# Kernel optimization log

Measured on AMD Instinct MI355X. Metric: run time of the kernel, lower is better.

## Reference

```python
import jax, jax.numpy as jnp
import numpy as np

N = 50000      # nodes
E = 1600000    # edges (avg degree 32)
D_IN = 128
HID = 64


def setup_inputs() -> dict:
    key = jax.random.key(0)
    ks = jax.random.split(key, 7)
    x = jax.random.normal(ks[0], (N, D_IN), dtype=jnp.float32)
    ei = jax.random.randint(ks[1], (2, E), 0, N, dtype=jnp.int32)
    ew = jax.random.uniform(ks[2], (E,), dtype=jnp.float32)
    # GCNConv linear weights (glorot-ish scale); lin has no bias, conv bias added post-aggregation
    W1 = jax.random.normal(ks[3], (HID, D_IN), dtype=jnp.float32) * (1.0 / np.sqrt(D_IN))
    b1 = jnp.zeros((HID,), dtype=jnp.float32)
    W2 = jax.random.normal(ks[4], (HID, HID), dtype=jnp.float32) * (1.0 / np.sqrt(HID))
    b2 = jnp.zeros((HID,), dtype=jnp.float32)
    return {"x": x, "ei": ei, "ew": ew, "W1": W1, "b1": b1, "W2": W2, "b2": b2}


def _gcn_conv(x, src, dst, ew_all, W, b, n_nodes):
    """PyG GCNConv: gcn_norm (self-loops already appended) + x@W.T, gather-scale-scatter, +b."""
    deg = jax.ops.segment_sum(ew_all, dst, num_segments=n_nodes)  # dst-side weighted degree
    dinv = jnp.where(deg > 0, jax.lax.rsqrt(deg), 0.0)            # deg^{-1/2}, inf->0
    norm = dinv[src] * ew_all * dinv[dst]                          # [E+N]
    h = x @ W.T                                                    # [N, hid]
    msg = h[src] * norm[:, None]                                   # gather + scale
    out = jax.ops.segment_sum(msg, dst, num_segments=n_nodes)     # scatter-add
    return out + b


def reference(x, ei, ew, W1, b1, W2, b2):
    n_nodes = x.shape[0]
    # add self loops once (fill value 1.0), shared by both conv layers
    loop = jnp.arange(n_nodes, dtype=ei.dtype)
    src = jnp.concatenate([ei[0], loop])
    dst = jnp.concatenate([ei[1], loop])
    ew_all = jnp.concatenate([ew, jnp.ones((n_nodes,), dtype=ew.dtype)])

    h1 = jax.nn.relu(_gcn_conv(x, src, dst, ew_all, W1, b1, n_nodes))
    # dropout is identity in eval mode
    h2 = _gcn_conv(h1, src, dst, ew_all, W2, b2, n_nodes)
    return h2 + h1
```

## Files before the change

### kernel.cpp

```cpp
#include <hip/hip_runtime.h>

#define HID 64
#define DIN 128
#define NBLK 512
#define CSH 14
#define CAP (1 << CSH)

typedef unsigned long long ull;
typedef unsigned short u16;

static __device__ __forceinline__ u16 f2bf(float f) {
  unsigned u = __float_as_uint(f);
  unsigned lsb = (u >> 16) & 1u;
  u += 0x7fffu + lsb;
  return (u16)(u >> 16);
}


__global__ __launch_bounds__(512) void k_build(const int* __restrict__ src,
                                               const int* __restrict__ dst,
                                               const float* __restrict__ ew,
                                               int* __restrict__ cursor,
                                               int2* __restrict__ bufA,
                                               int E, int NBC, int chunk,
                                               const float* __restrict__ W1,
                                               const float* __restrict__ W2,
                                               float* __restrict__ WT1,
                                               float* __restrict__ WT2) {
  int b = blockIdx.x, tid = threadIdx.x;
  if (b >= NBLK) {
    int idx = (b - NBLK) * 512 + tid;
    if (idx < DIN * 64) {
      int d = idx >> 6, j = idx & 63;
      WT1[idx] = W1[j * DIN + d];
    }
    int i2 = idx - DIN * 64;
    if (i2 >= 0 && i2 < HID * 64) {
      int d = i2 >> 6, j = i2 & 63;
      WT2[i2] = W2[j * HID + d];
    }
    return;
  }
  __shared__ int h[256];
  __shared__ int cur[256];
  if (tid < 256) h[tid] = 0;
  __syncthreads();
  int e0 = b * chunk, e1 = min(E, e0 + chunk);
  for (int e = e0 + tid; e < e1; e += 512) atomicAdd(&h[dst[e] >> 8], 1);
  __syncthreads();
  if (tid < 256) {
    int c = h[tid];
    int ofs = (c > 0) ? atomicAdd(&cursor[tid], c) : 0;
    cur[tid] = (tid << CSH) + ofs;
  }
  __syncthreads();
  for (int e = e0 + tid; e < e1; e += 512) {
    int s = src[e], d = dst[e];
    float w = ew[e];
    int p = atomicAdd(&cur[d >> 8], 1);
    bufA[p] = make_int2(__float_as_int(w), (int)(((unsigned)s << 16) | (unsigned)d));
  }
}


__global__ __launch_bounds__(512) void k_passB(const int2* __restrict__ bufA,
                                               const int* __restrict__ cursor,
                                               int2* __restrict__ bufB,
                                               int* __restrict__ offs,
                                               int* __restrict__ cnt,
                                               float* __restrict__ dinv,
                                               int NBC, int N) {
  int bin = blockIdx.x, tid = threadIdx.x;
  __shared__ int h2[256];
  __shared__ int cur[256];
  __shared__ float dg[256];
  int bbase = bin << CSH;
  int m = cursor[bin];
  if (tid < 256) { h2[tid] = 0; dg[tid] = 0.f; }
  __syncthreads();
  for (int i = tid; i < m; i += 512) {
    unsigned sd = (unsigned)bufA[bbase + i].y;
    atomicAdd(&h2[sd & 255], 1);
  }
  __syncthreads();
  int own = (tid < 256) ? h2[tid] : 0;
  for (int o = 1; o < 256; o <<= 1) {
    int u = 0;
    if (tid < 256 && tid >= o) u = h2[tid - o];
    __syncthreads();
    if (tid < 256) h2[tid] += u;
    __syncthreads();
  }
  int nd = (bin << 8) + tid;
  if (tid < 256) {
    int excl = h2[tid] - own;
    cur[tid] = excl;
    if (nd < N) { offs[nd] = bbase + excl; cnt[nd] = own; }
  }
  __syncthreads();
  for (int i = tid; i < m; i += 512) {
    int2 r = bufA[bbase + i];
    unsigned sd = (unsigned)r.y;
    int dl = (int)(sd & 255u);
    int p = atomicAdd(&cur[dl], 1);
    bufB[bbase + p] = r;
    atomicAdd(&dg[dl], __int_as_float(r.x));
  }
  __syncthreads();
  if (tid < 256 && nd < N) dinv[nd] = rsqrtf(1.0f + dg[tid]);
}


__global__ __launch_bounds__(256) void k_norm(int2* __restrict__ recs,
                                              const int* __restrict__ cursor,
                                              const float* __restrict__ dinv, int nslab) {
  int e = blockIdx.x * 256 + threadIdx.x;
  if (e < nslab && (e & (CAP - 1)) < cursor[e >> CSH]) {
    int2 r = recs[e];
    unsigned sd = (unsigned)r.y;
    int s = (int)(sd >> 16), d = (int)(sd & 0xffffu);
    float nrm = dinv[s] * __int_as_float(r.x) * dinv[d];
    recs[e] = make_int2(__float_as_int(nrm), s);
  }
}


template <int K>
__global__ __launch_bounds__(256) void k_gemm(const float* __restrict__ X,
                                              const float* __restrict__ WTg,
                                              u16* __restrict__ out, int n_nodes) {
  constexpr int PAD = 68;
  __shared__ float XT[64 * PAD];
  __shared__ float WL[64 * PAD];
  const int tid = threadIdx.x;
  const int n0 = blockIdx.x * 64;
  const int tx = tid & 15;
  const int ty = tid >> 4;
  float acc[4][4] = {{0.f}};

  for (int ph = 0; ph < K / 64; ++ph) {
    const int d0 = ph * 64;
    __syncthreads();
#pragma unroll
    for (int k = 0; k < 4; ++k) {
      int f = tid + k * 256;
      int r = f >> 4, q = f & 15;
      int n = n0 + r;
      float4 xv = (n < n_nodes)
        ? *reinterpret_cast<const float4*>(&X[(size_t)n * K + d0 + 4 * q])
        : make_float4(0.f, 0.f, 0.f, 0.f);
      *reinterpret_cast<float4*>(&XT[r * PAD + 4 * q]) = xv;
      float4 wv = *reinterpret_cast<const float4*>(&WTg[(size_t)(d0 + r) * 64 + 4 * q]);
      *reinterpret_cast<float4*>(&WL[r * PAD + 4 * q]) = wv;
    }
    __syncthreads();
#pragma unroll 4
    for (int dd = 0; dd < 64; dd += 4) {
      float4 xs[4], ws[4];
#pragma unroll
      for (int mi = 0; mi < 4; ++mi)
        xs[mi] = *reinterpret_cast<const float4*>(&XT[(4 * ty + mi) * PAD + dd]);
#pragma unroll
      for (int dk = 0; dk < 4; ++dk)
        ws[dk] = *reinterpret_cast<const float4*>(&WL[(dd + dk) * PAD + 4 * tx]);
#pragma unroll
      for (int mi = 0; mi < 4; ++mi) {
        float xm[4] = {xs[mi].x, xs[mi].y, xs[mi].z, xs[mi].w};
#pragma unroll
        for (int dk = 0; dk < 4; ++dk) {
          acc[mi][0] = fmaf(xm[dk], ws[dk].x, acc[mi][0]);
          acc[mi][1] = fmaf(xm[dk], ws[dk].y, acc[mi][1]);
          acc[mi][2] = fmaf(xm[dk], ws[dk].z, acc[mi][2]);
          acc[mi][3] = fmaf(xm[dk], ws[dk].w, acc[mi][3]);
        }
      }
    }
  }

#pragma unroll
  for (int mi = 0; mi < 4; ++mi) {
    int n = n0 + 4 * ty + mi;
    if (n < n_nodes) {
      ushort4 o = make_ushort4(f2bf(acc[mi][0]), f2bf(acc[mi][1]),
                               f2bf(acc[mi][2]), f2bf(acc[mi][3]));
      *reinterpret_cast<ushort4*>(&out[(size_t)n * HID + 4 * tx]) = o;
    }
  }
}


__device__ __forceinline__ void bfma8(const uint4& v, float w, float* a) {
  a[0] = fmaf(__uint_as_float(v.x << 16), w, a[0]);
  a[1] = fmaf(__uint_as_float(v.x & 0xffff0000u), w, a[1]);
  a[2] = fmaf(__uint_as_float(v.y << 16), w, a[2]);
  a[3] = fmaf(__uint_as_float(v.y & 0xffff0000u), w, a[3]);
  a[4] = fmaf(__uint_as_float(v.z << 16), w, a[4]);
  a[5] = fmaf(__uint_as_float(v.z & 0xffff0000u), w, a[5]);
  a[6] = fmaf(__uint_as_float(v.w << 16), w, a[6]);
  a[7] = fmaf(__uint_as_float(v.w & 0xffff0000u), w, a[7]);
}

__global__ __launch_bounds__(256) void k_agg(const u16* __restrict__ h,
                                             const int2* __restrict__ recs,
                                             const int* __restrict__ offs,
                                             const int* __restrict__ cnt,
                                             const float* __restrict__ dinv,
                                             const float* __restrict__ bias,
                                             const float* __restrict__ resid,
                                             float* __restrict__ out, int n_nodes, int mode) {
  int tid = threadIdx.x;
  int lane = tid & 63;
  int g = lane >> 3;
  int p8 = (lane & 7) * 8;
  int node = (blockIdx.x * 4 + (tid >> 6)) * 8 + g;
  if (node >= n_nodes) return;
  int beg = offs[node], end = beg + cnt[node];
  float di = dinv[node];

  float a[8], b[8];
  {
    uint4 v = *reinterpret_cast<const uint4*>(&h[(size_t)node * HID + p8]);
    float w = di * di;
    a[0] = __uint_as_float(v.x << 16) * w;
    a[1] = __uint_as_float(v.x & 0xffff0000u) * w;
    a[2] = __uint_as_float(v.y << 16) * w;
    a[3] = __uint_as_float(v.y & 0xffff0000u) * w;
    a[4] = __uint_as_float(v.z << 16) * w;
    a[5] = __uint_as_float(v.z & 0xffff0000u) * w;
    a[6] = __uint_as_float(v.w << 16) * w;
    a[7] = __uint_as_float(v.w & 0xffff0000u) * w;
#pragma unroll
    for (int j = 0; j < 8; ++j) b[j] = 0.f;
  }

  int i = beg;
  while (i + 8 <= end) {
    int2 r0 = recs[i];     int2 r1 = recs[i + 1];
    int2 r2 = recs[i + 2]; int2 r3 = recs[i + 3];
    int2 r4 = recs[i + 4]; int2 r5 = recs[i + 5];
    int2 r6 = recs[i + 6]; int2 r7 = recs[i + 7];
    uint4 v0 = *reinterpret_cast<const uint4*>(&h[(size_t)r0.y * HID + p8]);
    uint4 v1 = *reinterpret_cast<const uint4*>(&h[(size_t)r1.y * HID + p8]);
    uint4 v2 = *reinterpret_cast<const uint4*>(&h[(size_t)r2.y * HID + p8]);
    uint4 v3 = *reinterpret_cast<const uint4*>(&h[(size_t)r3.y * HID + p8]);
    uint4 v4 = *reinterpret_cast<const uint4*>(&h[(size_t)r4.y * HID + p8]);
    uint4 v5 = *reinterpret_cast<const uint4*>(&h[(size_t)r5.y * HID + p8]);
    uint4 v6 = *reinterpret_cast<const uint4*>(&h[(size_t)r6.y * HID + p8]);
    uint4 v7 = *reinterpret_cast<const uint4*>(&h[(size_t)r7.y * HID + p8]);
    bfma8(v0, __int_as_float(r0.x), a);
    bfma8(v1, __int_as_float(r1.x), b);
    bfma8(v2, __int_as_float(r2.x), a);
    bfma8(v3, __int_as_float(r3.x), b);
    bfma8(v4, __int_as_float(r4.x), a);
    bfma8(v5, __int_as_float(r5.x), b);
    bfma8(v6, __int_as_float(r6.x), a);
    bfma8(v7, __int_as_float(r7.x), b);
    i += 8;
  }
  if (i + 4 <= end) {
    int2 r0 = recs[i];     int2 r1 = recs[i + 1];
    int2 r2 = recs[i + 2]; int2 r3 = recs[i + 3];
    uint4 v0 = *reinterpret_cast<const uint4*>(&h[(size_t)r0.y * HID + p8]);
    uint4 v1 = *reinterpret_cast<const uint4*>(&h[(size_t)r1.y * HID + p8]);
    uint4 v2 = *reinterpret_cast<const uint4*>(&h[(size_t)r2.y * HID + p8]);
    uint4 v3 = *reinterpret_cast<const uint4*>(&h[(size_t)r3.y * HID + p8]);
    bfma8(v0, __int_as_float(r0.x), a);
    bfma8(v1, __int_as_float(r1.x), b);
    bfma8(v2, __int_as_float(r2.x), a);
    bfma8(v3, __int_as_float(r3.x), b);
    i += 4;
  }
  if (i + 2 <= end) {
    int2 r0 = recs[i];     int2 r1 = recs[i + 1];
    uint4 v0 = *reinterpret_cast<const uint4*>(&h[(size_t)r0.y * HID + p8]);
    uint4 v1 = *reinterpret_cast<const uint4*>(&h[(size_t)r1.y * HID + p8]);
    bfma8(v0, __int_as_float(r0.x), a);
    bfma8(v1, __int_as_float(r1.x), b);
    i += 2;
  }
  if (i < end) {
    int2 r0 = recs[i];
    uint4 v0 = *reinterpret_cast<const uint4*>(&h[(size_t)r0.y * HID + p8]);
    bfma8(v0, __int_as_float(r0.x), a);
  }

  float r[8];
#pragma unroll
  for (int j = 0; j < 8; ++j) r[j] = a[j] + b[j];
  float4 bb0 = *reinterpret_cast<const float4*>(&bias[p8]);
  float4 bb1 = *reinterpret_cast<const float4*>(&bias[p8 + 4]);
  r[0] += bb0.x; r[1] += bb0.y; r[2] += bb0.z; r[3] += bb0.w;
  r[4] += bb1.x; r[5] += bb1.y; r[6] += bb1.z; r[7] += bb1.w;
  if (mode == 0) {
#pragma unroll
    for (int j = 0; j < 8; ++j) r[j] = fmaxf(r[j], 0.f);
  } else {
    float4 rs0 = *reinterpret_cast<const float4*>(&resid[(size_t)node * HID + p8]);
    float4 rs1 = *reinterpret_cast<const float4*>(&resid[(size_t)node * HID + p8 + 4]);
    r[0] += rs0.x; r[1] += rs0.y; r[2] += rs0.z; r[3] += rs0.w;
    r[4] += rs1.x; r[5] += rs1.y; r[6] += rs1.z; r[7] += rs1.w;
  }
  *reinterpret_cast<float4*>(&out[(size_t)node * HID + p8]) =
      make_float4(r[0], r[1], r[2], r[3]);
  *reinterpret_cast<float4*>(&out[(size_t)node * HID + p8 + 4]) =
      make_float4(r[4], r[5], r[6], r[7]);
}


extern "C" void kernel_launch(void* const* d_in, const int* in_sizes, int n_in,
                              void* d_out, int out_size, void* d_ws, size_t ws_size,
                              hipStream_t stream) {
  const float* x  = (const float*)d_in[0];
  const int*   ei = (const int*)d_in[1];
  const float* ew = (const float*)d_in[2];
  const float* W1 = (const float*)d_in[3];
  const float* b1 = (const float*)d_in[4];
  const float* W2 = (const float*)d_in[5];
  const float* b2 = (const float*)d_in[6];
  float* out = (float*)d_out;

  const int N = in_sizes[0] / DIN;
  const int E = in_sizes[2];
  const int* src = ei;
  const int* dst = ei + E;

  const int NBC = (N + 255) >> 8;
  const int chunk = (E + NBLK - 1) / NBLK;
  const int nslab = NBC << CSH;

  char* p = (char*)d_ws;
  auto carve = [&](size_t bytes) {
    char* r = p;
    p += (bytes + 255) & ~(size_t)255;
    return r;
  };
  int*   cursor = (int*)carve(256 * 4);
  int*   offs   = (int*)carve((size_t)N * 4);
  int*   cnt    = (int*)carve((size_t)N * 4);
  float* dinv   = (float*)carve((size_t)N * 4);
  int2*  bufA   = (int2*)carve((size_t)nslab * 8);
  int2*  bufB   = (int2*)carve((size_t)nslab * 8);
  u16*   h      = (u16*)carve((size_t)N * HID * 2);
  float* h1     = (float*)carve((size_t)N * HID * 4);
  float* WT1    = (float*)carve((size_t)DIN * HID * 4);
  float* WT2    = (float*)carve((size_t)HID * HID * 4);

  int gblk = (N + 63) / 64;
  int ablk = (N + 31) / 32;
  int tblk = ((DIN + HID) * 64 + 511) / 512;

  hipMemsetAsync(cursor, 0, 256 * 4, stream);
  k_build<<<NBLK + tblk, 512, 0, stream>>>(src, dst, ew, cursor, bufA, E, NBC, chunk,
                                           W1, W2, WT1, WT2);
  k_passB<<<NBC, 512, 0, stream>>>(bufA, cursor, bufB, offs, cnt, dinv, NBC, N);
  k_norm<<<(nslab + 255) / 256, 256, 0, stream>>>(bufB, cursor, dinv, nslab);

  k_gemm<DIN><<<gblk, 256, 0, stream>>>(x, WT1, h, N);
  k_agg<<<ablk, 256, 0, stream>>>(h, bufB, offs, cnt, dinv, b1, nullptr, h1, N, 0);
  k_gemm<HID><<<gblk, 256, 0, stream>>>(h1, WT2, h, N);
  k_agg<<<ablk, 256, 0, stream>>>(h, bufB, offs, cnt, dinv, b2, h1, out, N, 1);
}
```

Measured before the change: 225.4 us.

## Fold degree normalization into GEMM output and aggregation epilogue, drop norm kernel

The per-edge normalization kernel is removed. The source-side dinv is now applied to h rows in the GEMM epilogue and the destination-side dinv is applied once per node after aggregation, so edge records carry only the raw weight and the source index. passB now runs with 1024 threads and keeps up to 16 records per thread in registers, so bufA is read once instead of twice. In the aggregation loop, one lane per 8-lane group loads each record and shares it with the rest of its group through shuffles. The trade-offs are a bf16 rounding of h after the dinv scaling, and a hard cap on bin size tied to 16×1024 records.

```diff
diff --git a/kernel.cpp b/kernel.cpp
--- a/kernel.cpp
+++ b/kernel.cpp
@@ -63,13 +63,13 @@
 }
 
 
-__global__ __launch_bounds__(512) void k_passB(const int2* __restrict__ bufA,
-                                               const int* __restrict__ cursor,
-                                               int2* __restrict__ bufB,
-                                               int* __restrict__ offs,
-                                               int* __restrict__ cnt,
-                                               float* __restrict__ dinv,
-                                               int NBC, int N) {
+__global__ __launch_bounds__(1024) void k_passB(const int2* __restrict__ bufA,
+                                                const int* __restrict__ cursor,
+                                                int2* __restrict__ bufB,
+                                                int* __restrict__ offs,
+                                                int* __restrict__ cnt,
+                                                float* __restrict__ dinv,
+                                                int NBC, int N) {
   int bin = blockIdx.x, tid = threadIdx.x;
   __shared__ int h2[256];
   __shared__ int cur[256];
@@ -78,9 +78,14 @@
   int m = cursor[bin];
   if (tid < 256) { h2[tid] = 0; dg[tid] = 0.f; }
   __syncthreads();
-  for (int i = tid; i < m; i += 512) {
-    unsigned sd = (unsigned)bufA[bbase + i].y;
-    atomicAdd(&h2[sd & 255], 1);
+  int2 rloc[16];
+#pragma unroll
+  for (int k = 0; k < 16; ++k) {
+    int i = tid + k * 1024;
+    if (i < m) {
+      rloc[k] = bufA[bbase + i];
+      atomicAdd(&h2[(unsigned)rloc[k].y & 255u], 1);
+    }
   }
   __syncthreads();
   int own = (tid < 256) ? h2[tid] : 0;
@@ -98,36 +103,27 @@
     if (nd < N) { offs[nd] = bbase + excl; cnt[nd] = own; }
   }
   __syncthreads();
-  for (int i = tid; i < m; i += 512) {
-    int2 r = bufA[bbase + i];
-    unsigned sd = (unsigned)r.y;
-    int dl = (int)(sd & 255u);
-    int p = atomicAdd(&cur[dl], 1);
-    bufB[bbase + p] = r;
-    atomicAdd(&dg[dl], __int_as_float(r.x));
+#pragma unroll
+  for (int k = 0; k < 16; ++k) {
+    int i = tid + k * 1024;
+    if (i < m) {
+      int2 r = rloc[k];
+      unsigned sd = (unsigned)r.y;
+      int dl = (int)(sd & 255u);
+      int p = atomicAdd(&cur[dl], 1);
+      bufB[bbase + p] = make_int2(r.x, (int)(sd >> 16));
+      atomicAdd(&dg[dl], __int_as_float(r.x));
+    }
   }
   __syncthreads();
   if (tid < 256 && nd < N) dinv[nd] = rsqrtf(1.0f + dg[tid]);
-}
-
-
-__global__ __launch_bounds__(256) void k_norm(int2* __restrict__ recs,
-                                              const int* __restrict__ cursor,
-                                              const float* __restrict__ dinv, int nslab) {
-  int e = blockIdx.x * 256 + threadIdx.x;
-  if (e < nslab && (e & (CAP - 1)) < cursor[e >> CSH]) {
-    int2 r = recs[e];
-    unsigned sd = (unsigned)r.y;
-    int s = (int)(sd >> 16), d = (int)(sd & 0xffffu);
-    float nrm = dinv[s] * __int_as_float(r.x) * dinv[d];
-    recs[e] = make_int2(__float_as_int(nrm), s);
-  }
 }
 
 
 template <int K>
 __global__ __launch_bounds__(256) void k_gemm(const float* __restrict__ X,
                                               const float* __restrict__ WTg,
+                                              const float* __restrict__ dinv,
                                               u16* __restrict__ out, int n_nodes) {
   constexpr int PAD = 68;
   __shared__ float XT[64 * PAD];
@@ -181,8 +177,9 @@
   for (int mi = 0; mi < 4; ++mi) {
     int n = n0 + 4 * ty + mi;
     if (n < n_nodes) {
-      ushort4 o = make_ushort4(f2bf(acc[mi][0]), f2bf(acc[mi][1]),
-                               f2bf(acc[mi][2]), f2bf(acc[mi][3]));
+      float dn = dinv[n];
+      ushort4 o = make_ushort4(f2bf(acc[mi][0] * dn), f2bf(acc[mi][1] * dn),
+                               f2bf(acc[mi][2] * dn), f2bf(acc[mi][3] * dn));
       *reinterpret_cast<ushort4*>(&out[(size_t)n * HID + 4 * tx]) = o;
     }
   }
@@ -220,41 +217,30 @@
   float a[8], b[8];
   {
     uint4 v = *reinterpret_cast<const uint4*>(&h[(size_t)node * HID + p8]);
-    float w = di * di;
-    a[0] = __uint_as_float(v.x << 16) * w;
-    a[1] = __uint_as_float(v.x & 0xffff0000u) * w;
-    a[2] = __uint_as_float(v.y << 16) * w;
-    a[3] = __uint_as_float(v.y & 0xffff0000u) * w;
-    a[4] = __uint_as_float(v.z << 16) * w;
-    a[5] = __uint_as_float(v.z & 0xffff0000u) * w;
-    a[6] = __uint_as_float(v.w << 16) * w;
-    a[7] = __uint_as_float(v.w & 0xffff0000u) * w;
+    a[0] = __uint_as_float(v.x << 16);
+    a[1] = __uint_as_float(v.x & 0xffff0000u);
+    a[2] = __uint_as_float(v.y << 16);
+    a[3] = __uint_as_float(v.y & 0xffff0000u);
+    a[4] = __uint_as_float(v.z << 16);
+    a[5] = __uint_as_float(v.z & 0xffff0000u);
+    a[6] = __uint_as_float(v.w << 16);
+    a[7] = __uint_as_float(v.w & 0xffff0000u);
 #pragma unroll
     for (int j = 0; j < 8; ++j) b[j] = 0.f;
   }
 
+  const int gb = lane & 56;
   int i = beg;
   while (i + 8 <= end) {
-    int2 r0 = recs[i];     int2 r1 = recs[i + 1];
-    int2 r2 = recs[i + 2]; int2 r3 = recs[i + 3];
-    int2 r4 = recs[i + 4]; int2 r5 = recs[i + 5];
-    int2 r6 = recs[i + 6]; int2 r7 = recs[i + 7];
-    uint4 v0 = *reinterpret_cast<const uint4*>(&h[(size_t)r0.y * HID + p8]);
-    uint4 v1 = *reinterpret_cast<const uint4*>(&h[(size_t)r1.y * HID + p8]);
-    uint4 v2 = *reinterpret_cast<const uint4*>(&h[(size_t)r2.y * HID + p8]);
-    uint4 v3 = *reinterpret_cast<const uint4*>(&h[(size_t)r3.y * HID + p8]);
-    uint4 v4 = *reinterpret_cast<const uint4*>(&h[(size_t)r4.y * HID + p8]);
-    uint4 v5 = *reinterpret_cast<const uint4*>(&h[(size_t)r5.y * HID + p8]);
-    uint4 v6 = *reinterpret_cast<const uint4*>(&h[(size_t)r6.y * HID + p8]);
-    uint4 v7 = *reinterpret_cast<const uint4*>(&h[(size_t)r7.y * HID + p8]);
-    bfma8(v0, __int_as_float(r0.x), a);
-    bfma8(v1, __int_as_float(r1.x), b);
-    bfma8(v2, __int_as_float(r2.x), a);
-    bfma8(v3, __int_as_float(r3.x), b);
-    bfma8(v4, __int_as_float(r4.x), a);
-    bfma8(v5, __int_as_float(r5.x), b);
-    bfma8(v6, __int_as_float(r6.x), a);
-    bfma8(v7, __int_as_float(r7.x), b);
+    ull rr = *reinterpret_cast<const ull*>(&recs[i + (lane & 7)]);
+#pragma unroll
+    for (int k = 0; k < 8; ++k) {
+      ull q = __shfl(rr, gb | k, 64);
+      float wk = __uint_as_float((unsigned)q);
+      int sk = (int)(q >> 32);
+      uint4 vk = *reinterpret_cast<const uint4*>(&h[(size_t)sk * HID + p8]);
+      bfma8(vk, wk, (k & 1) ? b : a);
+    }
     i += 8;
   }
   if (i + 4 <= end) {
@@ -286,7 +272,7 @@
 
   float r[8];
 #pragma unroll
-  for (int j = 0; j < 8; ++j) r[j] = a[j] + b[j];
+  for (int j = 0; j < 8; ++j) r[j] = (a[j] + b[j]) * di;
   float4 bb0 = *reinterpret_cast<const float4*>(&bias[p8]);
   float4 bb1 = *reinterpret_cast<const float4*>(&bias[p8 + 4]);
   r[0] += bb0.x; r[1] += bb0.y; r[2] += bb0.z; r[3] += bb0.w;
@@ -352,11 +338,10 @@
   hipMemsetAsync(cursor, 0, 256 * 4, stream);
   k_build<<<NBLK + tblk, 512, 0, stream>>>(src, dst, ew, cursor, bufA, E, NBC, chunk,
                                            W1, W2, WT1, WT2);
-  k_passB<<<NBC, 512, 0, stream>>>(bufA, cursor, bufB, offs, cnt, dinv, NBC, N);
-  k_norm<<<(nslab + 255) / 256, 256, 0, stream>>>(bufB, cursor, dinv, nslab);
-
-  k_gemm<DIN><<<gblk, 256, 0, stream>>>(x, WT1, h, N);
+  k_passB<<<NBC, 1024, 0, stream>>>(bufA, cursor, bufB, offs, cnt, dinv, NBC, N);
+
+  k_gemm<DIN><<<gblk, 256, 0, stream>>>(x, WT1, dinv, h, N);
   k_agg<<<ablk, 256, 0, stream>>>(h, bufB, offs, cnt, dinv, b1, nullptr, h1, N, 0);
-  k_gemm<HID><<<gblk, 256, 0, stream>>>(h1, WT2, h, N);
+  k_gemm<HID><<<gblk, 256, 0, stream>>>(h1, WT2, dinv, h, N);
   k_agg<<<ablk, 256, 0, stream>>>(h, bufB, offs, cnt, dinv, b2, h1, out, N, 1);
 }
```

Result: no change. 221.8 us (-1.6%).
